# Kernel optimization log

Measured on AMD Instinct MI355X. Metric: run time of the kernel, lower is better.

Reference implementation:

```python
import jax, jax.numpy as jnp
import numpy as np

T, B, H, L2, C = 1132, 128, 13, 100, 10  # seq, batch, hidden, total layers (2x50), classes


def setup_inputs() -> dict:
    key = jax.random.key(0)
    ks = jax.random.split(key, 7)
    s = 1.0 / np.sqrt(H)  # torch LSTM/Linear default init scale
    return {
        "input": jax.random.normal(ks[0], (B, T, H), jnp.float32),
        "w_ih": jax.random.uniform(ks[1], (L2, 4 * H, H), jnp.float32, -s, s),
        "w_hh": jax.random.uniform(ks[2], (L2, 4 * H, H), jnp.float32, -s, s),
        "b_ih": jax.random.uniform(ks[3], (L2, 4 * H), jnp.float32, -s, s),
        "b_hh": jax.random.uniform(ks[4], (L2, 4 * H), jnp.float32, -s, s),
        "w_lin": jax.random.uniform(ks[5], (C, T * H), jnp.float32, -1.0 / np.sqrt(T * H), 1.0 / np.sqrt(T * H)),
        "b_lin": jax.random.uniform(ks[6], (C,), jnp.float32, -1.0 / np.sqrt(T * H), 1.0 / np.sqrt(T * H)),
    }


def _lstm_stack(x, w_ih, w_hh, b_ih, b_hh):
    # x: [T, B, H]; weights stacked over layers: [L, 4H, H], biases [L, 4H]
    def layer(x, params):
        Wih, Whh, bih, bhh = params
        # input contribution for all timesteps at once (one big GEMM)
        pre = jnp.einsum('tbf,gf->tbg', x, Wih) + bih + bhh  # [T, B, 4H]

        def step(carry, p):
            h, c = carry
            g = p + h @ Whh.T  # [B, 4H]
            i, f, gg, o = jnp.split(g, 4, axis=-1)  # torch gate order: i,f,g,o
            c = jax.nn.sigmoid(f) * c + jax.nn.sigmoid(i) * jnp.tanh(gg)
            h = jax.nn.sigmoid(o) * jnp.tanh(c)
            return (h, c), h

        h0 = jnp.zeros((x.shape[1], Whh.shape[1]), x.dtype)
        _, hs = jax.lax.scan(step, (h0, h0), pre)
        return hs, None

    x, _ = jax.lax.scan(layer, x, (w_ih, w_hh, b_ih, b_hh))
    return x


def reference(input, w_ih, w_hh, b_ih, b_hh, w_lin, b_lin):
    x = jnp.transpose(input, (1, 0, 2))  # [T, B, H] (time-major for scan)
    x = _lstm_stack(x, w_ih, w_hh, b_ih, b_hh)
    x = jnp.transpose(x, (1, 0, 2)).reshape(input.shape[0], -1)  # [B, T*H]
    logits = x @ w_lin.T + b_lin
    return jax.nn.softmax(logits, axis=1)
```

## Files before the change

### kernel.cpp

```cpp
#include <hip/hip_runtime.h>
#include <stdint.h>

#define T_SEQ  1132
#define BATCH  128
#define HID    13
#define G4     52
#define NLAYER 100
#define NPIPE  8
#define LPW    4
#define NWGP   25
#define NTHR   384
#define CH     4
#define NCH    283
#define RCL    4
#define RC     8
#define NCLS   10
#define FEAT   (T_SEQ*HID)
#define L2E    1.44269504f

#define CHUNK_U32 (CH*256)
#define FLAG_BYTES 65536
#define RING_U32_PER_WG ((size_t)RC * CHUNK_U32)
#define RING_BYTES ((size_t)(NPIPE*NWGP) * RING_U32_PER_WG * 4)

typedef float  f32x4 __attribute__((ext_vector_type(4)));
typedef __fp16 f16x4 __attribute__((ext_vector_type(4)));
typedef unsigned int u32x4 __attribute__((ext_vector_type(4)));

struct HL { f16x4 h; f16x4 l; };

__device__ __forceinline__ void f16split(float x, __fp16& hi, __fp16& lo) {
  hi = (__fp16)x;
  lo = (__fp16)(x - (float)hi);
}

__device__ __forceinline__ void lspin_ge(int* p, int need) {
  int v = __hip_atomic_load(p, __ATOMIC_ACQUIRE, __HIP_MEMORY_SCOPE_WORKGROUP);
  while (v < need) {
    __builtin_amdgcn_s_sleep(1);
    v = __hip_atomic_load(p, __ATOMIC_ACQUIRE, __HIP_MEMORY_SCOPE_WORKGROUP);
  }
}
__device__ __forceinline__ void gspin_ge(int* p, int need) {
  int v = __hip_atomic_load(p, __ATOMIC_RELAXED, __HIP_MEMORY_SCOPE_AGENT);
  while (v < need) {
    __builtin_amdgcn_s_sleep(1);
    v = __hip_atomic_load(p, __ATOMIC_RELAXED, __HIP_MEMORY_SCOPE_AGENT);
  }
}

__global__ __launch_bounds__(NTHR) void lstm_pipeline(
    const float* __restrict__ xin,
    const float* __restrict__ w_ih,
    const float* __restrict__ w_hh,
    const float* __restrict__ b_ih,
    const float* __restrict__ b_hh,
    int*      flags,
    uint32_t* ring,
    float*    act)
{
  const int wg   = blockIdx.x;
  const int pp   = wg / NWGP;
  const int wgi  = wg - pp * NWGP;
  const int tid  = threadIdx.x;
  const int lane = tid & 63;
  const int nt   = tid >> 6;
  const int quad = lane >> 4;
  const int b15  = lane & 15;
  const bool lastWG = (wgi == NWGP - 1);

  __shared__ __align__(16) uint32_t sXP[LPW][RCL][CH][256];
  __shared__ __align__(16) uint32_t sOutR[RCL][CH][256];
  __shared__ int sProg[LPW];
  __shared__ int sCons[LPW];
  __shared__ int sProgOut;
  __shared__ int sConsOut;

  int* flReadySelf = flags + ((pp * NWGP + wgi) * 2 + 0) * 16;
  int* flProgSelf  = flags + ((pp * NWGP + wgi) * 2 + 1) * 16;
  int* flReadyPrev = (wgi > 0) ? flags + ((pp * NWGP + wgi - 1) * 2 + 0) * 16 : flags;
  int* flProgNext  = (!lastWG) ? flags + ((pp * NWGP + wgi + 1) * 2 + 1) * 16 : flags;

  if (lane == 0) {
    if (nt == LPW + 1)
      __hip_atomic_store(flReadySelf, 0, __ATOMIC_RELAXED, __HIP_MEMORY_SCOPE_AGENT);
    if (nt == LPW)
      __hip_atomic_store(flProgSelf, 0, __ATOMIC_RELAXED, __HIP_MEMORY_SCOPE_AGENT);
  }
  if (tid < LPW) { sProg[tid] = 0; sCons[tid] = 0; }
  if (tid == 0) { sProgOut = 0; sConsOut = 0; }
  __syncthreads();

  if (nt < LPW) {
    const int l = wgi * LPW + nt;
    const bool lastL = (l == NLAYER - 1);

    f16x4 Axh[4], Axl[4], Ahh[4], Ahl[4];
    f32x4 biasv[4];
    #pragma unroll
    for (int mt = 0; mt < 4; ++mt) {
      const float gsc = (mt == 2) ? (2.0f * L2E) : (-L2E);
      #pragma unroll
      for (int jj = 0; jj < 4; ++jj) {
        int k = quad * 4 + jj;
        float wx = 0.f, wh = 0.f;
        if (b15 < HID && k < HID) {
          int g = mt * HID + b15;
          wx = w_ih[(size_t)(l * G4 + g) * HID + k];
          wh = w_hh[(size_t)(l * G4 + g) * HID + k];
        }
        wx *= gsc; wh *= gsc;
        __fp16 hi, lo;
        f16split(wx, hi, lo); Axh[mt][jj] = hi; Axl[mt][jj] = lo;
        f16split(wh, hi, lo); Ahh[mt][jj] = hi; Ahl[mt][jj] = lo;
      }
      #pragma unroll
      for (int r = 0; r < 4; ++r) {
        int jt = quad * 4 + r;
        biasv[mt][r] = (jt < HID)
            ? gsc * (b_ih[l * G4 + mt * HID + jt] + b_hh[l * G4 + mt * HID + jt]) : 0.f;
      }
    }

    f16x4 Bhh = (f16x4)0, Bhl = (f16x4)0;
    float cst[4] = {0.f, 0.f, 0.f, 0.f};

    #pragma unroll 1
    for (int ci = 0; ci < NCH; ++ci) {
      const int slot = ci & (RCL - 1);

      lspin_ge(&sProg[nt], ci + 1);
      if (ci + 1 - RCL > 0) {
        if (nt < LPW - 1) lspin_ge(&sCons[nt + 1], ci + 1 - RCL);
        else              lspin_ge(&sConsOut,       ci + 1 - RCL);
      }

      f32x4 ax[CH][4];
      #pragma unroll
      for (int s = 0; s < CH; ++s) {
        u32x4 bx = *(const u32x4*)&sXP[nt][slot][s][lane * 4];
        HL z = __builtin_bit_cast(HL, bx);
        #pragma unroll
        for (int mt = 0; mt < 4; ++mt) {
          f32x4 a = biasv[mt];
          a = __builtin_amdgcn_mfma_f32_16x16x16f16(Axh[mt], z.h, a, 0, 0, 0);
          a = __builtin_amdgcn_mfma_f32_16x16x16f16(Axl[mt], z.h, a, 0, 0, 0);
          a = __builtin_amdgcn_mfma_f32_16x16x16f16(Axh[mt], z.l, a, 0, 0, 0);
          ax[s][mt] = a;
        }
      }
      if (lane == 0)
        __hip_atomic_store(&sCons[nt], ci + 1, __ATOMIC_RELEASE, __HIP_MEMORY_SCOPE_WORKGROUP);

      #pragma unroll
      for (int s = 0; s < CH; ++s) {
        f32x4 acc[4];
        #pragma unroll
        for (int mt = 0; mt < 4; ++mt) {
          f32x4 a = ax[s][mt];
          a = __builtin_amdgcn_mfma_f32_16x16x16f16(Ahh[mt], Bhh, a, 0, 0, 0);
          a = __builtin_amdgcn_mfma_f32_16x16x16f16(Ahl[mt], Bhh, a, 0, 0, 0);
          a = __builtin_amdgcn_mfma_f32_16x16x16f16(Ahh[mt], Bhl, a, 0, 0, 0);
          acc[mt] = a;
        }
        float hnv[4];
        #pragma unroll
        for (int r = 0; r < 4; ++r) {
          float eA = __builtin_amdgcn_exp2f(acc[0][r]);
          float eC = __builtin_amdgcn_exp2f(acc[1][r]);
          float eB = __builtin_amdgcn_exp2f(acc[2][r]);
          float eD = __builtin_amdgcn_exp2f(acc[3][r]);
          float ta = 1.0f + eA, tb = 1.0f + eB, tc = 1.0f + eC;
          float p  = ta * tb;
          float ri = __builtin_amdgcn_rcpf(p * tc);
          float num = fmaf((eB - 1.0f) * tc, 2.0f * L2E, cst[r] * p);
          float cn = num * ri;
          cst[r] = cn;
          float eE = __builtin_amdgcn_exp2f(fminf(cn, 100.0f));
          float r2 = __builtin_amdgcn_rcpf((eE + 1.0f) * (1.0f + eD));
          float h  = (eE - 1.0f) * r2;
          hnv[r] = h;
          __fp16 hi, lo; f16split(h, hi, lo);
          Bhh[r] = hi; Bhl[r] = lo;
        }
        if (nt < LPW - 1) {
          HL o; o.h = Bhh; o.l = Bhl;
          *(u32x4*)&sXP[nt + 1][slot][s][lane * 4] = __builtin_bit_cast(u32x4, o);
        } else if (!lastL) {
          HL o; o.h = Bhh; o.l = Bhl;
          *(u32x4*)&sOutR[slot][s][lane * 4] = __builtin_bit_cast(u32x4, o);
        } else {
          u32x4 w;
          #pragma unroll
          for (int r = 0; r < 4; ++r) w[r] = __float_as_uint(hnv[r]);
          *(u32x4*)&sOutR[slot][s][lane * 4] = w;
        }
      }

      if (lane == 0) {
        if (nt < LPW - 1)
          __hip_atomic_store(&sProg[nt + 1], ci + 1, __ATOMIC_RELEASE, __HIP_MEMORY_SCOPE_WORKGROUP);
        else
          __hip_atomic_store(&sProgOut, ci + 1, __ATOMIC_RELEASE, __HIP_MEMORY_SCOPE_WORKGROUP);
      }
    }
  } else if (nt == LPW) {
    const uint32_t* ringprev = ring + (size_t)(pp * NWGP + wgi - 1) * RING_U32_PER_WG;
    const size_t    xrow     = (size_t)(pp * 16 + b15) * (T_SEQ * HID);

    #pragma unroll 1
    for (int cin = 0; cin < NCH; ++cin) {
      const int slot = cin & (RCL - 1);
      if (cin + 1 - RCL > 0) lspin_ge(&sCons[0], cin + 1 - RCL);

      if (wgi > 0) {
        gspin_ge(flReadyPrev, cin + 1);
        const uint32_t* src = ringprev + (size_t)(cin & (RC - 1)) * CHUNK_U32;
        uint32_t v[CH][4];
        #pragma unroll
        for (int s = 0; s < CH; ++s)
          #pragma unroll
          for (int w = 0; w < 4; ++w)
            v[s][w] = __hip_atomic_load(&src[s * 256 + lane * 4 + w],
                                        __ATOMIC_RELAXED, __HIP_MEMORY_SCOPE_AGENT);
        #pragma unroll
        for (int s = 0; s < CH; ++s) {
          u32x4 q = { v[s][0], v[s][1], v[s][2], v[s][3] };
          *(u32x4*)&sXP[0][slot][s][lane * 4] = q;
        }
        asm volatile("s_waitcnt vmcnt(0)" ::: "memory");
        if (lane == 0)
          __hip_atomic_store(flProgSelf, cin + 1, __ATOMIC_RELAXED, __HIP_MEMORY_SCOPE_AGENT);
      } else {
        const int t0 = cin * CH;
        #pragma unroll
        for (int s = 0; s < CH; ++s) {
          HL o;
          #pragma unroll
          for (int jj = 0; jj < 4; ++jj) {
            int k = quad * 4 + jj;
            float v = (k < HID) ? xin[xrow + (size_t)(t0 + s) * HID + k] : 0.f;
            __fp16 hi, lo; f16split(v, hi, lo);
            o.h[jj] = hi; o.l[jj] = lo;
          }
          *(u32x4*)&sXP[0][slot][s][lane * 4] = __builtin_bit_cast(u32x4, o);
        }
      }
      if (lane == 0)
        __hip_atomic_store(&sProg[0], cin + 1, __ATOMIC_RELEASE, __HIP_MEMORY_SCOPE_WORKGROUP);
    }
  } else {
    uint32_t* ringmine = ring + (size_t)(pp * NWGP + wgi) * RING_U32_PER_WG;

    #pragma unroll 1
    for (int cout = 0; cout < NCH; ++cout) {
      const int slot = cout & (RCL - 1);
      lspin_ge(&sProgOut, cout + 1);

      if (!lastWG) {
        if (cout + 1 - RC > 0) gspin_ge(flProgNext, cout + 1 - RC);
        uint32_t* dst = ringmine + (size_t)(cout & (RC - 1)) * CHUNK_U32;
        #pragma unroll
        for (int s = 0; s < CH; ++s) {
          u32x4 v = *(const u32x4*)&sOutR[slot][s][lane * 4];
          #pragma unroll
          for (int w = 0; w < 4; ++w)
            __hip_atomic_store(&dst[s * 256 + lane * 4 + w], v[w],
                               __ATOMIC_RELAXED, __HIP_MEMORY_SCOPE_AGENT);
        }
        asm volatile("s_waitcnt vmcnt(0)" ::: "memory");
        if (lane == 0) {
          __hip_atomic_store(flReadySelf, cout + 1, __ATOMIC_RELAXED, __HIP_MEMORY_SCOPE_AGENT);
          __hip_atomic_store(&sConsOut, cout + 1, __ATOMIC_RELEASE, __HIP_MEMORY_SCOPE_WORKGROUP);
        }
      } else {
        const int t0 = cout * CH;
        #pragma unroll
        for (int s = 0; s < CH; ++s) {
          u32x4 v = *(const u32x4*)&sOutR[slot][s][lane * 4];
          float* dst = act + (size_t)(t0 + s) * (BATCH * HID)
                     + (size_t)(pp * 16 + b15) * HID + quad * 4;
          #pragma unroll
          for (int r = 0; r < 4; ++r)
            if (quad * 4 + r < HID) dst[r] = __uint_as_float(v[r]);
        }
        if (lane == 0)
          __hip_atomic_store(&sConsOut, cout + 1, __ATOMIC_RELEASE, __HIP_MEMORY_SCOPE_WORKGROUP);
      }
    }
  }
}

__global__ __launch_bounds__(256) void linear_softmax(
    const float* __restrict__ act,
    const float* __restrict__ w_lin,
    const float* __restrict__ b_lin,
    float* __restrict__ out)
{
  const int b   = blockIdx.x;
  const int tid = threadIdx.x;
  float accv[NCLS];
  #pragma unroll
  for (int c = 0; c < NCLS; ++c) accv[c] = 0.f;

  for (int i = tid; i < FEAT; i += 256) {
    int t = i / HID; int jj = i - t * HID;
    float a = act[(size_t)t * (BATCH * HID) + b * HID + jj];
    #pragma unroll
    for (int c = 0; c < NCLS; ++c)
      accv[c] += a * w_lin[(size_t)c * FEAT + i];
  }

  __shared__ float red[NCLS][256];
  #pragma unroll
  for (int c = 0; c < NCLS; ++c) red[c][tid] = accv[c];
  __syncthreads();
  for (int off = 128; off > 0; off >>= 1) {
    if (tid < off) {
      #pragma unroll
      for (int c = 0; c < NCLS; ++c) red[c][tid] += red[c][tid + off];
    }
    __syncthreads();
  }
  if (tid == 0) {
    float lg[NCLS]; float mx = -1e30f;
    #pragma unroll
    for (int c = 0; c < NCLS; ++c) { lg[c] = red[c][0] + b_lin[c]; mx = fmaxf(mx, lg[c]); }
    float sum = 0.f;
    #pragma unroll
    for (int c = 0; c < NCLS; ++c) { lg[c] = __expf(lg[c] - mx); sum += lg[c]; }
    float inv = 1.0f / sum;
    #pragma unroll
    for (int c = 0; c < NCLS; ++c) out[b * NCLS + c] = lg[c] * inv;
  }
}

extern "C" void kernel_launch(void* const* d_in, const int* in_sizes, int n_in,
                              void* d_out, int out_size, void* d_ws, size_t ws_size,
                              hipStream_t stream) {
  const float* xin  = (const float*)d_in[0];
  const float* wih  = (const float*)d_in[1];
  const float* whh  = (const float*)d_in[2];
  const float* bih  = (const float*)d_in[3];
  const float* bhh  = (const float*)d_in[4];
  const float* wlin = (const float*)d_in[5];
  const float* blin = (const float*)d_in[6];

  char*     ws    = (char*)d_ws;
  int*      flags = (int*)ws;
  uint32_t* ring  = (uint32_t*)(ws + FLAG_BYTES);
  float*    act   = (float*)(ws + FLAG_BYTES + RING_BYTES);

  lstm_pipeline<<<NPIPE * NWGP, NTHR, 0, stream>>>(xin, wih, whh, bih, bhh, flags, ring, act);
  linear_softmax<<<BATCH, 256, 0, stream>>>(act, wlin, blin, (float*)d_out);
}
```

Measured before the change: 919.7 us.

## Signal layer progress per timestep instead of per chunk within workgroup pipeline

Switches the intra-workgroup layer-to-layer progress counters from chunk granularity to per-timestep granularity. Each layer wave now publishes its output after every timestep and computes the next timestep's input projection right after the recurrent MFMAs. This lets the next layer start on step s without waiting for the whole 4-step chunk, shortening pipeline fill and per-chunk latency across the 4 stacked layers. In exchange there are more LDS atomic stores and spin-waits per chunk, and the consumer-release store is moved to the end of the chunk.

Result: faster. 874.7 us (-4.9%).

```diff
diff --git a/kernel.cpp b/kernel.cpp
--- a/kernel.cpp
+++ b/kernel.cpp
@@ -128,17 +128,17 @@
     #pragma unroll 1
     for (int ci = 0; ci < NCH; ++ci) {
       const int slot = ci & (RCL - 1);
-
-      lspin_ge(&sProg[nt], ci + 1);
+      const int base = ci * CH;
+
       if (ci + 1 - RCL > 0) {
         if (nt < LPW - 1) lspin_ge(&sCons[nt + 1], ci + 1 - RCL);
         else              lspin_ge(&sConsOut,       ci + 1 - RCL);
       }
 
-      f32x4 ax[CH][4];
-      #pragma unroll
-      for (int s = 0; s < CH; ++s) {
-        u32x4 bx = *(const u32x4*)&sXP[nt][slot][s][lane * 4];
+      lspin_ge(&sProg[nt], base + 1);
+      f32x4 axc[4];
+      {
+        u32x4 bx = *(const u32x4*)&sXP[nt][slot][0][lane * 4];
         HL z = __builtin_bit_cast(HL, bx);
         #pragma unroll
         for (int mt = 0; mt < 4; ++mt) {
@@ -146,23 +146,36 @@
           a = __builtin_amdgcn_mfma_f32_16x16x16f16(Axh[mt], z.h, a, 0, 0, 0);
           a = __builtin_amdgcn_mfma_f32_16x16x16f16(Axl[mt], z.h, a, 0, 0, 0);
           a = __builtin_amdgcn_mfma_f32_16x16x16f16(Axh[mt], z.l, a, 0, 0, 0);
-          ax[s][mt] = a;
-        }
-      }
-      if (lane == 0)
-        __hip_atomic_store(&sCons[nt], ci + 1, __ATOMIC_RELEASE, __HIP_MEMORY_SCOPE_WORKGROUP);
+          axc[mt] = a;
+        }
+      }
 
       #pragma unroll
       for (int s = 0; s < CH; ++s) {
         f32x4 acc[4];
         #pragma unroll
         for (int mt = 0; mt < 4; ++mt) {
-          f32x4 a = ax[s][mt];
+          f32x4 a = axc[mt];
           a = __builtin_amdgcn_mfma_f32_16x16x16f16(Ahh[mt], Bhh, a, 0, 0, 0);
           a = __builtin_amdgcn_mfma_f32_16x16x16f16(Ahl[mt], Bhh, a, 0, 0, 0);
           a = __builtin_amdgcn_mfma_f32_16x16x16f16(Ahh[mt], Bhl, a, 0, 0, 0);
           acc[mt] = a;
         }
+
+        if (s < CH - 1) {
+          lspin_ge(&sProg[nt], base + s + 2);
+          u32x4 bx = *(const u32x4*)&sXP[nt][slot][s + 1][lane * 4];
+          HL z = __builtin_bit_cast(HL, bx);
+          #pragma unroll
+          for (int mt = 0; mt < 4; ++mt) {
+            f32x4 a = biasv[mt];
+            a = __builtin_amdgcn_mfma_f32_16x16x16f16(Axh[mt], z.h, a, 0, 0, 0);
+            a = __builtin_amdgcn_mfma_f32_16x16x16f16(Axl[mt], z.h, a, 0, 0, 0);
+            a = __builtin_amdgcn_mfma_f32_16x16x16f16(Axh[mt], z.l, a, 0, 0, 0);
+            axc[mt] = a;
+          }
+        }
+
         float hnv[4];
         #pragma unroll
         for (int r = 0; r < 4; ++r) {
@@ -186,23 +199,25 @@
         if (nt < LPW - 1) {
           HL o; o.h = Bhh; o.l = Bhl;
           *(u32x4*)&sXP[nt + 1][slot][s][lane * 4] = __builtin_bit_cast(u32x4, o);
+          if (lane == 0)
+            __hip_atomic_store(&sProg[nt + 1], base + s + 1, __ATOMIC_RELEASE, __HIP_MEMORY_SCOPE_WORKGROUP);
         } else if (!lastL) {
           HL o; o.h = Bhh; o.l = Bhl;
           *(u32x4*)&sOutR[slot][s][lane * 4] = __builtin_bit_cast(u32x4, o);
+          if (lane == 0)
+            __hip_atomic_store(&sProgOut, base + s + 1, __ATOMIC_RELEASE, __HIP_MEMORY_SCOPE_WORKGROUP);
         } else {
           u32x4 w;
           #pragma unroll
           for (int r = 0; r < 4; ++r) w[r] = __float_as_uint(hnv[r]);
           *(u32x4*)&sOutR[slot][s][lane * 4] = w;
-        }
-      }
-
-      if (lane == 0) {
-        if (nt < LPW - 1)
-          __hip_atomic_store(&sProg[nt + 1], ci + 1, __ATOMIC_RELEASE, __HIP_MEMORY_SCOPE_WORKGROUP);
-        else
-          __hip_atomic_store(&sProgOut, ci + 1, __ATOMIC_RELEASE, __HIP_MEMORY_SCOPE_WORKGROUP);
-      }
+          if (lane == 0)
+            __hip_atomic_store(&sProgOut, base + s + 1, __ATOMIC_RELEASE, __HIP_MEMORY_SCOPE_WORKGROUP);
+        }
+      }
+
+      if (lane == 0)
+        __hip_atomic_store(&sCons[nt], ci + 1, __ATOMIC_RELEASE, __HIP_MEMORY_SCOPE_WORKGROUP);
     }
   } else if (nt == LPW) {
     const uint32_t* ringprev = ring + (size_t)(pp * NWGP + wgi - 1) * RING_U32_PER_WG;
@@ -247,7 +262,7 @@
         }
       }
       if (lane == 0)
-        __hip_atomic_store(&sProg[0], cin + 1, __ATOMIC_RELEASE, __HIP_MEMORY_SCOPE_WORKGROUP);
+        __hip_atomic_store(&sProg[0], (cin + 1) * CH, __ATOMIC_RELEASE, __HIP_MEMORY_SCOPE_WORKGROUP);
     }
   } else {
     uint32_t* ringmine = ring + (size_t)(pp * NWGP + wgi) * RING_U32_PER_WG;
@@ -255,7 +270,7 @@
     #pragma unroll 1
     for (int cout = 0; cout < NCH; ++cout) {
       const int slot = cout & (RCL - 1);
-      lspin_ge(&sProgOut, cout + 1);
+      lspin_ge(&sProgOut, (cout + 1) * CH);
 
       if (!lastWG) {
         if (cout + 1 - RC > 0) gspin_ge(flProgNext, cout + 1 - RC);
```
